# Performance work log

Measured on AMD Instinct MI355X. Metric: run time of the kernel, lower is better.

## Reference

```python
import jax, jax.numpy as jnp
import numpy as np

# positions 0,1 = input tensor dims; positions 2,3 = output tensor dims (single entity type)

def _set_partitions(elems):
    if not elems:
        yield []
        return
    first, rest = elems[0], elems[1:]
    for p in _set_partitions(rest):
        for i in range(len(p)):
            yield p[:i] + [p[i] + [first]] + p[i + 1:]
    # note: generator above already covers merging; add singleton case

def _all_set_partitions(elems):
    if not elems:
        return [[]]
    first, rest = elems[0], elems[1:]
    out = []
    for p in _all_set_partitions(rest):
        for i in range(len(p)):
            out.append(p[:i] + [p[i] + [first]] + p[i + 1:])
        out.append([[first]] + p)
    return out

PARTITIONS = _all_set_partitions([0, 1, 2, 3])  # Bell(4) = 15 equivariant partitions


def _apply_partition(X, part, eye, ones):
    """Dense equivalent of diag -> pool -> broadcast -> undiag -> reindex for one partition.
    X: [b, c, n, n]. Returns [b, c, n, n]."""
    pos2blk = {p: bi for bi, blk in enumerate(part) for p in blk}
    blk_letter = {bi: 'defg'[bi] for bi in range(len(part))}
    # step 1: diag (repeated letters) + pool (letters dropped from output)
    in_sub = 'bc' + blk_letter[pos2blk[0]] + blk_letter[pos2blk[1]]
    keep = [bi for bi, blk in enumerate(part)
            if any(p < 2 for p in blk) and any(p >= 2 for p in blk)]
    z_sub = 'bc' + ''.join(blk_letter[bi] for bi in keep)
    Z = jnp.einsum(f'{in_sub}->{z_sub}', X)
    # step 2: broadcast + diag-embed into output positions via eye/ones factors
    out_letter = {2: 'p', 3: 'q'}
    operands, subs = [Z], [z_sub]
    for bi, blk in enumerate(part):
        outpos = [p for p in blk if p >= 2]
        if not outpos:
            continue
        if any(p < 2 for p in blk):  # block tied to a surviving input dim
            for p in outpos:
                operands.append(eye)
                subs.append(blk_letter[bi] + out_letter[p])
        else:  # pure broadcast block
            first = outpos[0]
            operands.append(ones)
            subs.append(out_letter[first])
            for p in outpos[1:]:
                operands.append(eye)
                subs.append(out_letter[first] + out_letter[p])
    return jnp.einsum(','.join(subs) + '->bcpq', *operands)


def setup_inputs() -> dict:
    key = jax.random.key(0)
    k1, k2 = jax.random.split(key)
    B, C_IN, C_OUT, N = 4, 96, 96, 256
    stdv = 0.1 / np.sqrt(C_IN)
    X_in = jax.random.normal(k1, (B, C_IN, N, N), dtype=jnp.float32)
    Y_in = jnp.zeros((B, C_IN, N, N), dtype=jnp.float32)  # only provides output shape
    weights = jax.random.uniform(k2, (15, C_IN, C_OUT), minval=-stdv, maxval=stdv, dtype=jnp.float32)
    bias = jnp.ones((1,), dtype=jnp.float32)
    return {'X_in': X_in, 'Y_in': Y_in, 'weights': weights, 'bias': bias}


def reference(X_in, Y_in, weights, bias):
    n = X_in.shape[-1]
    eye = jnp.eye(n, dtype=X_in.dtype)
    ones = jnp.ones((n,), dtype=X_in.dtype)
    Y = None
    for i, part in enumerate(PARTITIONS):
        Yp = _apply_partition(X_in, part, eye, ones)          # [b, c_in, n, n]
        Yp = jnp.einsum('bcpq,co->bopq', Yp, weights[i])       # channel linear
        Y = Yp if Y is None else Y + Yp
    return Y + bias[0]
```

## Files before the change

### kernel.cpp

```cpp
#include <hip/hip_runtime.h>
#include <hip/hip_bf16.h>

#define NN 256
#define CIN 96
#define COUT 96
#define BB 4
#define NBC (BB * CIN)
#define SEG (NBC * NN)

typedef __attribute__((ext_vector_type(8))) short short8;
typedef __attribute__((ext_vector_type(4))) float f32x4;

__device__ __forceinline__ float waveReduceSum(float v) {
    #pragma unroll
    for (int m = 32; m >= 1; m >>= 1) v += __shfl_xor(v, m, 64);
    return v;
}

__device__ __forceinline__ unsigned int packbf2(float lo, float hi) {
    __hip_bfloat162 h = __float22bfloat162_rn(make_float2(lo, hi));
    unsigned int u;
    __builtin_memcpy(&u, &h, 4);
    return u;
}

__device__ __forceinline__ short8 u4_to_s8(uint4 u) {
    short8 r;
    __builtin_memcpy(&r, &u, 16);
    return r;
}

__global__ __launch_bounds__(256) void k_aux(const float* __restrict__ X,
                                             float* __restrict__ rows,
                                             float* __restrict__ diag,
                                             float* __restrict__ colsP,
                                             float* __restrict__ TSp) {
    const int blk = blockIdx.x;
    const int ch = blk & 3, bc = blk >> 2;
    const float* Xp = X + (size_t)bc * (NN * NN) + (size_t)ch * 64 * NN;
    const int tid = threadIdx.x;
    const int w = tid >> 6, lane = tid & 63;

    __shared__ float colPart[4][NN];
    __shared__ float sred[4];

    float4 csum = make_float4(0.f, 0.f, 0.f, 0.f);
    #pragma unroll
    for (int b2 = 0; b2 < 2; ++b2) {
        float4 v[8];
        #pragma unroll
        for (int j = 0; j < 8; ++j) {
            const int r = w * 16 + b2 * 8 + j;
            v[j] = *(const float4*)(Xp + (size_t)r * NN + lane * 4);
        }
        #pragma unroll
        for (int j = 0; j < 8; ++j) {
            csum.x += v[j].x; csum.y += v[j].y; csum.z += v[j].z; csum.w += v[j].w;
            float rs = waveReduceSum(v[j].x + v[j].y + v[j].z + v[j].w);
            if (lane == 0)
                rows[(size_t)bc * NN + ch * 64 + w * 16 + b2 * 8 + j] = rs;
        }
    }
    *(float4*)&colPart[w][lane * 4] = csum;

    if (w == 0) {
        float dv = Xp[(size_t)lane * NN + ch * 64 + lane];
        diag[(size_t)bc * NN + ch * 64 + lane] = dv;
        float t1 = waveReduceSum(dv);
        if (lane == 0) TSp[(ch * NBC + bc) * 2 + 0] = t1;
    }
    __syncthreads();

    float col = colPart[0][tid] + colPart[1][tid] + colPart[2][tid] + colPart[3][tid];
    colsP[(size_t)ch * SEG + (size_t)bc * NN + tid] = col;
    float s1 = waveReduceSum(col);
    if (lane == 0) sred[w] = s1;
    __syncthreads();
    if (tid == 0)
        TSp[(ch * NBC + bc) * 2 + 1] = sred[0] + sred[1] + sred[2] + sred[3];
}

__global__ __launch_bounds__(256) void k_sum(const float* __restrict__ colsP,
                                             const float* __restrict__ TSp,
                                             const float* __restrict__ W,
                                             float* __restrict__ cols,
                                             float* __restrict__ TSa,
                                             uint4* __restrict__ wpk) {
    const int blk = blockIdx.x;
    if (blk < NBC) {
        const int bc = blk;
        const int p = threadIdx.x;
        const size_t base = (size_t)bc * NN + p;
        cols[base] = colsP[0 * (size_t)SEG + base] + colsP[1 * (size_t)SEG + base]
                   + colsP[2 * (size_t)SEG + base] + colsP[3 * (size_t)SEG + base];
        if (p < 2)
            TSa[bc * 2 + p] = TSp[(0 * NBC + bc) * 2 + p] + TSp[(1 * NBC + bc) * 2 + p]
                            + TSp[(2 * NBC + bc) * 2 + p] + TSp[(3 * NBC + bc) * 2 + p];
    } else {
        const int e = (blk - NBC) * 256 + threadIdx.x;
        if (e < 2304) {
            const int lane = e & 63;
            const int pair = (e >> 6) & 1;
            const int sm = e >> 7;
            const int col = lane & 15, g = lane >> 4;
            const int s = sm / 6, m = sm - s * 6;
            const int o = m * 16 + col;
            const int cb = 32 * s + 8 * g;
            const float* wsrc = W + (pair ? 6 : 8) * CIN * COUT + (size_t)cb * COUT + o;
            uint4 v;
            v.x = packbf2(wsrc[0 * COUT], wsrc[1 * COUT]);
            v.y = packbf2(wsrc[2 * COUT], wsrc[3 * COUT]);
            v.z = packbf2(wsrc[4 * COUT], wsrc[5 * COUT]);
            v.w = packbf2(wsrc[6 * COUT], wsrc[7 * COUT]);
            wpk[e] = v;
        }
    }
}

__global__ __launch_bounds__(512) void k_pqg(const float* __restrict__ W,
                                             const float* __restrict__ rows,
                                             const float* __restrict__ cols,
                                             const float* __restrict__ diag,
                                             const float* __restrict__ TSa,
                                             const float* __restrict__ bias,
                                             float* __restrict__ Pw,
                                             float* __restrict__ Qw,
                                             float* __restrict__ Gw) {
    const int bo = blockIdx.x;
    const int b = bo / COUT, o = bo % COUT;
    const int half = threadIdx.x >> 8;
    const int p = threadIdx.x & 255;

    __shared__ float red[5][256];

    float P = 0.f, Q = 0.f, G = 0.f, s = 0.f, gs = 0.f;
    const int cbeg = half * 48, cend = cbeg + 48;
    for (int c = cbeg; c < cend; ++c) {
        const int bcq = b * CIN + c;
        const size_t base = (size_t)bcq * NN;
        float r  = rows[base + p];
        float cl = cols[base + p];
        float dg = diag[base + p];
        const float* wp = W + c * COUT + o;
        #define WI(i) wp[(i) * CIN * COUT]
        P += WI(12) * r + WI(7)  * cl + WI(5) * dg;
        Q += WI(13) * r + WI(10) * cl + WI(9) * dg;
        G += WI(3)  * r + WI(1)  * cl + WI(0) * dg;
        float Tv = TSa[bcq * 2 + 0];
        float Sv = TSa[bcq * 2 + 1];
        s  += WI(11) * Tv + WI(14) * Sv;
        gs += WI(2)  * Tv + WI(4)  * Sv;
        #undef WI
    }
    if (half == 1) {
        red[0][p] = P; red[1][p] = Q; red[2][p] = G; red[3][p] = s; red[4][p] = gs;
    }
    __syncthreads();
    if (half == 0) {
        P += red[0][p]; Q += red[1][p]; G += red[2][p]; s += red[3][p]; gs += red[4][p];
        const size_t ob = (size_t)bo * NN;
        Pw[ob + p] = P + s + bias[0];
        Qw[ob + p] = Q;
        Gw[ob + p] = G + gs;
    }
}

#define XPLANE 324

__global__ __launch_bounds__(512, 1) void k_main(const float* __restrict__ X,
                                                 const uint4* __restrict__ wpk,
                                                 const float* __restrict__ Pw,
                                                 const float* __restrict__ Qw,
                                                 const float* __restrict__ Gw,
                                                 float* __restrict__ Y) {
    __shared__ __align__(16) unsigned int XAs[16 * XPLANE];
    __shared__ __align__(16) unsigned int XBs[16 * XPLANE];
    __shared__ __align__(16) uint4 Wf[2304];

    const int orig = blockIdx.x + 16 * (blockIdx.y + 16 * blockIdx.z);
    const int work = (orig & 7) * 128 + (orig >> 3);
    const int tq = work & 15, tp = (work >> 4) & 15, b = work >> 8;

    const int tid = threadIdx.x;
    const int w = tid >> 6, lane = tid & 63;
    const int sp = lane >> 2, sq4 = (lane & 3) * 4;
    const int col = lane & 15, g = lane >> 4;

    #pragma unroll
    for (int i = tid; i < 2304; i += 512) Wf[i] = wpk[i];

    f32x4 acc[6][2];
    #pragma unroll
    for (int m = 0; m < 6; ++m) {
        acc[m][0] = f32x4{0.f, 0.f, 0.f, 0.f};
        acc[m][1] = f32x4{0.f, 0.f, 0.f, 0.f};
    }

    const float* Xb  = X + (size_t)b * CIN * NN * NN;
    const float* G1  = Xb + (size_t)(tp * 16) * NN + tq * 16;
    const float* G2  = Xb + (size_t)(tq * 16) * NN + tp * 16;

    const int cw0 = w, cw1 = w + 8;

    float4 a00, a01, b00, b01;
    float4 a10, a11, b10, b11;

    #define LOADG(C0) { \
        const size_t cb0 = (size_t)((C0) + 2 * cw0) * (NN * NN); \
        const size_t cb1 = (size_t)((C0) + 2 * cw1) * (NN * NN); \
        const float* pa0 = G1 + cb0 + sp * NN + sq4; \
        a00 = *(const float4*)pa0; \
        a01 = *(const float4*)(pa0 + NN * NN); \
        const float* pb0 = G2 + cb0 + sp * NN + sq4; \
        b00 = *(const float4*)pb0; \
        b01 = *(const float4*)(pb0 + NN * NN); \
        const float* pa1 = G1 + cb1 + sp * NN + sq4; \
        a10 = *(const float4*)pa1; \
        a11 = *(const float4*)(pa1 + NN * NN); \
        const float* pb1 = G2 + cb1 + sp * NN + sq4; \
        b10 = *(const float4*)pb1; \
        b11 = *(const float4*)(pb1 + NN * NN); }

    LOADG(0);

    #pragma unroll
    for (int s = 0; s < 3; ++s) {
        __syncthreads();

        {
            uint4 pk;
            pk.x = packbf2(a00.x, a01.x);
            pk.y = packbf2(a00.y, a01.y);
            pk.z = packbf2(a00.z, a01.z);
            pk.w = packbf2(a00.w, a01.w);
            *(uint4*)&XAs[cw0 * XPLANE + sp * 20 + sq4] = pk;
            pk.x = packbf2(a10.x, a11.x);
            pk.y = packbf2(a10.y, a11.y);
            pk.z = packbf2(a10.z, a11.z);
            pk.w = packbf2(a10.w, a11.w);
            *(uint4*)&XAs[cw1 * XPLANE + sp * 20 + sq4] = pk;
            unsigned int* dB0 = &XBs[cw0 * XPLANE + sp];
            dB0[(sq4 + 0) * 20] = packbf2(b00.x, b01.x);
            dB0[(sq4 + 1) * 20] = packbf2(b00.y, b01.y);
            dB0[(sq4 + 2) * 20] = packbf2(b00.z, b01.z);
            dB0[(sq4 + 3) * 20] = packbf2(b00.w, b01.w);
            unsigned int* dB1 = &XBs[cw1 * XPLANE + sp];
            dB1[(sq4 + 0) * 20] = packbf2(b10.x, b11.x);
            dB1[(sq4 + 1) * 20] = packbf2(b10.y, b11.y);
            dB1[(sq4 + 2) * 20] = packbf2(b10.z, b11.z);
            dB1[(sq4 + 3) * 20] = packbf2(b10.w, b11.w);
        }
        __syncthreads();

        if (s < 2) LOADG(32 * (s + 1));

        const unsigned int* xab = &XAs[4 * g * XPLANE + w * 20 + col];
        const unsigned int* xbb = &XBs[4 * g * XPLANE + w * 20 + col];
        uint4 u;
        u.x = xab[0]; u.y = xab[XPLANE]; u.z = xab[2 * XPLANE]; u.w = xab[3 * XPLANE];
        short8 xd0 = u4_to_s8(u);
        u.x = xab[160]; u.y = xab[XPLANE + 160]; u.z = xab[2 * XPLANE + 160]; u.w = xab[3 * XPLANE + 160];
        short8 xd1 = u4_to_s8(u);
        u.x = xbb[0]; u.y = xbb[XPLANE]; u.z = xbb[2 * XPLANE]; u.w = xbb[3 * XPLANE];
        short8 xt0 = u4_to_s8(u);
        u.x = xbb[160]; u.y = xbb[XPLANE + 160]; u.z = xbb[2 * XPLANE + 160]; u.w = xbb[3 * XPLANE + 160];
        short8 xt1 = u4_to_s8(u);

        const uint4* wb = &Wf[s * 768 + lane];
        #define MSTEP(M) { \
            short8 w8f = u4_to_s8(wb[(M) * 128]); \
            short8 w6f = u4_to_s8(wb[(M) * 128 + 64]); \
            acc[M][0] = __builtin_amdgcn_mfma_f32_16x16x32_bf16(xd0, w8f, acc[M][0], 0, 0, 0); \
            acc[M][0] = __builtin_amdgcn_mfma_f32_16x16x32_bf16(xt0, w6f, acc[M][0], 0, 0, 0); \
            acc[M][1] = __builtin_amdgcn_mfma_f32_16x16x32_bf16(xd1, w8f, acc[M][1], 0, 0, 0); \
            acc[M][1] = __builtin_amdgcn_mfma_f32_16x16x32_bf16(xt1, w6f, acc[M][1], 0, 0, 0); }
        MSTEP(0)
        MSTEP(1)
        MSTEP(2)
        MSTEP(3)
        MSTEP(4)
        MSTEP(5)
        #undef MSTEP
    }
    #undef LOADG

    const int p0 = tp * 16 + w;
    const int q4 = tq * 16 + g * 4;
    const bool diagblk = (tp == tq);
    #pragma unroll
    for (int m = 0; m < 6; ++m) {
        const int o = m * 16 + col;
        const size_t ob = (size_t)(b * COUT + o) * NN;
        const float4 qf = *(const float4*)&Qw[ob + q4];
        #pragma unroll
        for (int rr = 0; rr < 2; ++rr) {
            const int p = p0 + rr * 8;
            const float pv = Pw[ob + p];
            float4 out;
            out.x = acc[m][rr][0] + pv + qf.x;
            out.y = acc[m][rr][1] + pv + qf.y;
            out.z = acc[m][rr][2] + pv + qf.z;
            out.w = acc[m][rr][3] + pv + qf.w;
            if (diagblk) {
                const float gv = Gw[ob + p];
                const int d = (p & 15) - g * 4;
                if (d == 0) out.x += gv;
                else if (d == 1) out.y += gv;
                else if (d == 2) out.z += gv;
                else if (d == 3) out.w += gv;
            }
            *(float4*)&Y[(ob + p) * NN + q4] = out;
        }
    }
}

extern "C" void kernel_launch(void* const* d_in, const int* in_sizes, int n_in,
                              void* d_out, int out_size, void* d_ws, size_t ws_size,
                              hipStream_t stream) {
    const float* X    = (const float*)d_in[0];
    const float* W    = (const float*)d_in[2];
    const float* bias = (const float*)d_in[3];
    float* Y = (float*)d_out;

    float* ws    = (float*)d_ws;
    float* rows  = ws;
    float* diag  = ws + (size_t)SEG;
    float* colsP = ws + 2 * (size_t)SEG;
    float* Pw    = ws + 6 * (size_t)SEG;
    float* Qw    = ws + 7 * (size_t)SEG;
    float* Gw    = ws + 8 * (size_t)SEG;
    float* TSp   = ws + 9 * (size_t)SEG;
    float* TSa   = ws + 9 * (size_t)SEG + 4096;
    float* cols  = ws + 10 * (size_t)SEG;
    uint4* wpk   = (uint4*)(ws + 11 * (size_t)SEG);

    k_aux<<<NBC * 4, 256, 0, stream>>>(X, rows, diag, colsP, TSp);
    k_sum<<<NBC + 9, 256, 0, stream>>>(colsP, TSp, W, cols, TSa, wpk);
    k_pqg<<<BB * COUT, 512, 0, stream>>>(W, rows, cols, diag, TSa, bias, Pw, Qw, Gw);
    k_main<<<dim3(16, 16, BB), 512, 0, stream>>>(X, wpk, Pw, Qw, Gw, Y);
}
```

Before: 111.3 us.

## Stream packed weights per stage in k_main and split k_pqg blocks

```diff
diff --git a/kernel.cpp b/kernel.cpp
--- a/kernel.cpp
+++ b/kernel.cpp
@@ -117,7 +117,7 @@
     }
 }
 
-__global__ __launch_bounds__(512) void k_pqg(const float* __restrict__ W,
+__global__ __launch_bounds__(256) void k_pqg(const float* __restrict__ W,
                                              const float* __restrict__ rows,
                                              const float* __restrict__ cols,
                                              const float* __restrict__ diag,
@@ -126,12 +126,14 @@
                                              float* __restrict__ Pw,
                                              float* __restrict__ Qw,
                                              float* __restrict__ Gw) {
-    const int bo = blockIdx.x;
+    const int blk = blockIdx.x;
+    const int bo = blk >> 1, ph = blk & 1;
     const int b = bo / COUT, o = bo % COUT;
-    const int half = threadIdx.x >> 8;
-    const int p = threadIdx.x & 255;
-
-    __shared__ float red[5][256];
+    const int half = threadIdx.x >> 7;
+    const int pl = threadIdx.x & 127;
+    const int p = ph * 128 + pl;
+
+    __shared__ float red[5][128];
 
     float P = 0.f, Q = 0.f, G = 0.f, s = 0.f, gs = 0.f;
     const int cbeg = half * 48, cend = cbeg + 48;
@@ -153,11 +155,11 @@
         #undef WI
     }
     if (half == 1) {
-        red[0][p] = P; red[1][p] = Q; red[2][p] = G; red[3][p] = s; red[4][p] = gs;
+        red[0][pl] = P; red[1][pl] = Q; red[2][pl] = G; red[3][pl] = s; red[4][pl] = gs;
     }
     __syncthreads();
     if (half == 0) {
-        P += red[0][p]; Q += red[1][p]; G += red[2][p]; s += red[3][p]; gs += red[4][p];
+        P += red[0][pl]; Q += red[1][pl]; G += red[2][pl]; s += red[3][pl]; gs += red[4][pl];
         const size_t ob = (size_t)bo * NN;
         Pw[ob + p] = P + s + bias[0];
         Qw[ob + p] = Q;
@@ -175,7 +177,7 @@
                                                  float* __restrict__ Y) {
     __shared__ __align__(16) unsigned int XAs[16 * XPLANE];
     __shared__ __align__(16) unsigned int XBs[16 * XPLANE];
-    __shared__ __align__(16) uint4 Wf[2304];
+    __shared__ __align__(16) uint4 Ws[768];
 
     const int orig = blockIdx.x + 16 * (blockIdx.y + 16 * blockIdx.z);
     const int work = (orig & 7) * 128 + (orig >> 3);
@@ -186,9 +188,6 @@
     const int sp = lane >> 2, sq4 = (lane & 3) * 4;
     const int col = lane & 15, g = lane >> 4;
 
-    #pragma unroll
-    for (int i = tid; i < 2304; i += 512) Wf[i] = wpk[i];
-
     f32x4 acc[6][2];
     #pragma unroll
     for (int m = 0; m < 6; ++m) {
@@ -204,6 +203,7 @@
 
     float4 a00, a01, b00, b01;
     float4 a10, a11, b10, b11;
+    uint4 wr0, wr1 = {};
 
     #define LOADG(C0) { \
         const size_t cb0 = (size_t)((C0) + 2 * cw0) * (NN * NN); \
@@ -221,12 +221,19 @@
         b10 = *(const float4*)pb1; \
         b11 = *(const float4*)(pb1 + NN * NN); }
 
+    #define LOADW(S) { \
+        wr0 = wpk[(S) * 768 + tid]; \
+        if (tid < 256) wr1 = wpk[(S) * 768 + 512 + tid]; }
+
+    LOADW(0);
     LOADG(0);
 
     #pragma unroll
     for (int s = 0; s < 3; ++s) {
         __syncthreads();
 
+        Ws[tid] = wr0;
+        if (tid < 256) Ws[512 + tid] = wr1;
         {
             uint4 pk;
             pk.x = packbf2(a00.x, a01.x);
@@ -252,7 +259,10 @@
         }
         __syncthreads();
 
-        if (s < 2) LOADG(32 * (s + 1));
+        if (s < 2) {
+            LOADG(32 * (s + 1));
+            LOADW(s + 1);
+        }
 
         const unsigned int* xab = &XAs[4 * g * XPLANE + w * 20 + col];
         const unsigned int* xbb = &XBs[4 * g * XPLANE + w * 20 + col];
@@ -266,7 +276,7 @@
         u.x = xbb[160]; u.y = xbb[XPLANE + 160]; u.z = xbb[2 * XPLANE + 160]; u.w = xbb[3 * XPLANE + 160];
         short8 xt1 = u4_to_s8(u);
 
-        const uint4* wb = &Wf[s * 768 + lane];
+        const uint4* wb = &Ws[lane];
         #define MSTEP(M) { \
             short8 w8f = u4_to_s8(wb[(M) * 128]); \
             short8 w6f = u4_to_s8(wb[(M) * 128 + 64]); \
@@ -283,6 +293,7 @@
         #undef MSTEP
     }
     #undef LOADG
+    #undef LOADW
 
     const int p0 = tp * 16 + w;
     const int q4 = tq * 16 + g * 4;
@@ -336,6 +347,6 @@
 
     k_aux<<<NBC * 4, 256, 0, stream>>>(X, rows, diag, colsP, TSp);
     k_sum<<<NBC + 9, 256, 0, stream>>>(colsP, TSp, W, cols, TSa, wpk);
-    k_pqg<<<BB * COUT, 512, 0, stream>>>(W, rows, cols, diag, TSa, bias, Pw, Qw, Gw);
+    k_pqg<<<BB * COUT * 2, 256, 0, stream>>>(W, rows, cols, diag, TSa, bias, Pw, Qw, Gw);
     k_main<<<dim3(16, 16, BB), 512, 0, stream>>>(X, wpk, Pw, Qw, Gw, Y);
 }
```

New measurement: 113.6 us. 1.02x slower.
